# Kernel optimization log

Measured on AMD Instinct MI355X. Metric: run time of the kernel, lower is better.

The kernel has to match this reference:

```python
import jax, jax.numpy as jnp
import numpy as np

BATCH, NODES, CH_IN, CH_OUT, N_EXPERTS = 8, 8192, 128, 128, 64

def setup_inputs() -> dict:
    key = jax.random.key(0)
    kx, kw, ks = jax.random.split(key, 3)
    x = jax.random.normal(kx, (BATCH, NODES, CH_IN), dtype=jnp.float32)
    # std = fan_in**-0.5 per self_init
    W = jax.random.normal(kw, (N_EXPERTS, CH_OUT, CH_IN), dtype=jnp.float32) * (CH_IN ** -0.5)
    sel = jax.random.randint(ks, (NODES,), 0, N_EXPERTS, dtype=jnp.int64)
    return {"x": x, "sel": sel, "W": W}

def reference(x, sel, W):
    # x: (b, n, j), W[sel]: (n, i, j) -> out: (b, n, i)
    Wsel = W[sel]  # gather a (ch_out, ch_in) matrix per node
    return jnp.einsum('bnj,nij->bni', x, Wsel)
```

## Files before the change

kernel.cpp:

```cpp
#include <hip/hip_runtime.h>
#include <hip/hip_bf16.h>

#define BATCH   8
#define NODES   8192
#define CH      128
#define NEXP    64
#define TN      16
#define MAXP    (NODES + NEXP * TN)
#define NTILES  (MAXP / TN)

typedef __attribute__((ext_vector_type(8))) short bf16x8;
typedef __attribute__((ext_vector_type(4))) float f32x4;

__device__ __forceinline__ short f2bf(float f) {
    union { float f; unsigned u; } v; v.f = f;
    unsigned r = (v.u + 0x7fffu + ((v.u >> 16) & 1u)) >> 16;
    return (short)r;
}

__device__ __forceinline__ bf16x8 cvt8(f32x4 lo, f32x4 hi) {
    bf16x8 r;
    r[0] = f2bf(lo[0]); r[1] = f2bf(lo[1]); r[2] = f2bf(lo[2]); r[3] = f2bf(lo[3]);
    r[4] = f2bf(hi[0]); r[5] = f2bf(hi[1]); r[6] = f2bf(hi[2]); r[7] = f2bf(hi[3]);
    return r;
}

__global__ __launch_bounds__(256)
void prep_kernel(const int* __restrict__ sel, const float* __restrict__ W,
                 short* __restrict__ Wbf, int* __restrict__ sorted)
{
    const int e = blockIdx.x;
    const int t = threadIdx.x;

    {
        const float* ws = W   + (size_t)e * CH * CH;
        short*       wd = Wbf + (size_t)e * CH * CH;
        #pragma unroll
        for (int i = 0; i < 8; ++i) {
            int idx = (i * 256 + t) * 8;
            f32x4 lo = *reinterpret_cast<const f32x4*>(ws + idx);
            f32x4 hi = *reinterpret_cast<const f32x4*>(ws + idx + 4);
            *reinterpret_cast<bf16x8*>(wd + idx) = cvt8(lo, hi);
        }
    }

    __shared__ int cnt[NEXP];
    __shared__ int s_off, s_cnt, cursor;
    if (t < NEXP) cnt[t] = 0;
    if (t == 0) cursor = 0;
    __syncthreads();

    int myv[NODES / 256];
    #pragma unroll
    for (int i = 0; i < NODES / 256; ++i) {
        myv[i] = sel[i * 256 + t];
        atomicAdd(&cnt[myv[i]], 1);
    }
    __syncthreads();

    if (t == 0) {
        int off = 0, myoff = 0;
        for (int ee = 0; ee < NEXP; ++ee) {
            if (ee == e) myoff = off;
            off += (cnt[ee] + TN - 1) & ~(TN - 1);
        }
        s_off = myoff;
        s_cnt = cnt[e];
    }
    __syncthreads();

    const int off = s_off, myc = s_cnt;
    const int pad = (myc + TN - 1) & ~(TN - 1);

    for (int i = myc + t; i < pad; i += 256) sorted[off + i] = -1;

    if (e == NEXP - 1) {
        for (int i = off + pad + t; i < MAXP; i += 256) sorted[i] = -1;
    }

    #pragma unroll
    for (int i = 0; i < NODES / 256; ++i) {
        if (myv[i] == e) {
            int pos = atomicAdd(&cursor, 1);
            sorted[off + pos] = i * 256 + t;
        }
    }
}

__global__ __launch_bounds__(256)
void gemm_kernel(const float* __restrict__ x, const int* __restrict__ sel,
                 const short* __restrict__ Wbf, float* __restrict__ out,
                 const int* __restrict__ sorted)
{
    __shared__ int s_nodes[TN];
    __shared__ int s_expert;

    const int tid  = threadIdx.x;
    const int tile = blockIdx.x;

    if (tid < TN) s_nodes[tid] = sorted[tile * TN + tid];
    if (tid == 0) {
        int n0 = sorted[tile * TN];
        s_expert = (n0 >= 0) ? sel[n0] : -1;
    }
    __syncthreads();

    const int e = s_expert;
    if (e < 0) return;

    const int wave = tid >> 6;
    const int lane = tid & 63;
    const int m16  = lane & 15;
    const int quad = lane >> 4;

    const float* xrow[2];
    #pragma unroll
    for (int rt = 0; rt < 2; ++rt) {
        int r    = wave * 32 + rt * 16 + m16;
        int node = s_nodes[r >> 3];
        int b    = r & 7;
        int nd   = (node >= 0) ? node : 0;
        xrow[rt] = x + ((size_t)(b * NODES + nd)) * CH;
    }
    const short* wbase = Wbf + (size_t)e * CH * CH;

    f32x4 acc[2][8];
    #pragma unroll
    for (int rt = 0; rt < 2; ++rt)
        #pragma unroll
        for (int ct = 0; ct < 8; ++ct)
            acc[rt][ct] = (f32x4){0.f, 0.f, 0.f, 0.f};

    #pragma unroll
    for (int kk = 0; kk < 4; ++kk) {
        const int k0 = kk * 32 + quad * 8;

        bf16x8 afrag[2];
        #pragma unroll
        for (int rt = 0; rt < 2; ++rt) {
            const float* p = xrow[rt] + k0;
            f32x4 lo = *reinterpret_cast<const f32x4*>(p);
            f32x4 hi = *reinterpret_cast<const f32x4*>(p + 4);
            afrag[rt] = cvt8(lo, hi);
        }

        #pragma unroll
        for (int ct = 0; ct < 8; ++ct) {
            bf16x8 bfrag = *reinterpret_cast<const bf16x8*>(
                wbase + (size_t)(ct * 16 + m16) * CH + k0);
            acc[0][ct] = __builtin_amdgcn_mfma_f32_16x16x32_bf16(
                             afrag[0], bfrag, acc[0][ct], 0, 0, 0);
            acc[1][ct] = __builtin_amdgcn_mfma_f32_16x16x32_bf16(
                             afrag[1], bfrag, acc[1][ct], 0, 0, 0);
        }
    }

    #pragma unroll
    for (int rt = 0; rt < 2; ++rt) {
        #pragma unroll
        for (int reg = 0; reg < 4; ++reg) {
            int r    = wave * 32 + rt * 16 + quad * 4 + reg;
            int node = s_nodes[r >> 3];
            if (node < 0) continue;
            int b = r & 7;
            float* orow = out + ((size_t)(b * NODES + node)) * CH;
            #pragma unroll
            for (int ct = 0; ct < 8; ++ct)
                orow[ct * 16 + m16] = acc[rt][ct][reg];
        }
    }
}

extern "C" void kernel_launch(void* const* d_in, const int* in_sizes, int n_in,
                              void* d_out, int out_size, void* d_ws, size_t ws_size,
                              hipStream_t stream)
{
    const float* x   = (const float*)d_in[0];
    const int*   sel = (const int*)  d_in[1];
    const float* W   = (const float*)d_in[2];
    float*       out = (float*)d_out;

    short* Wbf   = (short*)d_ws;
    int*   sorted = (int*)((char*)d_ws + (size_t)NEXP * CH * CH * sizeof(short));

    prep_kernel<<<NEXP, 256, 0, stream>>>(sel, W, Wbf, sorted);
    gemm_kernel<<<NTILES, 256, 0, stream>>>(x, sel, Wbf, out, sorted);
}
```

Baseline: 114.4 us.

## Spread weight conversion over more blocks, parallel-scan offsets, and use 512-thread GEMM tiles

The prep kernel now launches 256 blocks so the fp32-to-bf16 weight conversion is spread across more CUs. Per-wave histograms cut LDS atomic contention, and a wave-level shuffle scan replaces the serial offset loop. The GEMM kernel uses 8 waves of 16 rows each instead of 4 waves of 32 rows, which halves per-thread accumulator registers and adds parallelism. Scalar rounding is replaced by the compiler's __bf16 conversion, which may lower to hardware convert instructions. Each B fragment is now reused for one MFMA instead of two, so more waves load the same weight data.

After: 124.3 us. +8.7%, slower.

```diff
diff --git a/kernel.cpp b/kernel.cpp
--- a/kernel.cpp
+++ b/kernel.cpp
@@ -1,5 +1,4 @@
 #include <hip/hip_runtime.h>
-#include <hip/hip_bf16.h>
 
 #define BATCH   8
 #define NODES   8192
@@ -12,16 +11,13 @@
 typedef __attribute__((ext_vector_type(8))) short bf16x8;
 typedef __attribute__((ext_vector_type(4))) float f32x4;
 
-__device__ __forceinline__ short f2bf(float f) {
-    union { float f; unsigned u; } v; v.f = f;
-    unsigned r = (v.u + 0x7fffu + ((v.u >> 16) & 1u)) >> 16;
-    return (short)r;
-}
-
 __device__ __forceinline__ bf16x8 cvt8(f32x4 lo, f32x4 hi) {
     bf16x8 r;
-    r[0] = f2bf(lo[0]); r[1] = f2bf(lo[1]); r[2] = f2bf(lo[2]); r[3] = f2bf(lo[3]);
-    r[4] = f2bf(hi[0]); r[5] = f2bf(hi[1]); r[6] = f2bf(hi[2]); r[7] = f2bf(hi[3]);
+    #pragma unroll
+    for (int i = 0; i < 4; ++i) {
+        r[i]     = (short)__builtin_bit_cast(unsigned short, static_cast<__bf16>(lo[i]));
+        r[i + 4] = (short)__builtin_bit_cast(unsigned short, static_cast<__bf16>(hi[i]));
+    }
     return r;
 }
 
@@ -29,14 +25,14 @@
 void prep_kernel(const int* __restrict__ sel, const float* __restrict__ W,
                  short* __restrict__ Wbf, int* __restrict__ sorted)
 {
-    const int e = blockIdx.x;
     const int t = threadIdx.x;
 
     {
-        const float* ws = W   + (size_t)e * CH * CH;
-        short*       wd = Wbf + (size_t)e * CH * CH;
+        const size_t base = (size_t)blockIdx.x * (CH * CH / 4);
+        const float* ws = W   + base;
+        short*       wd = Wbf + base;
         #pragma unroll
-        for (int i = 0; i < 8; ++i) {
+        for (int i = 0; i < 2; ++i) {
             int idx = (i * 256 + t) * 8;
             f32x4 lo = *reinterpret_cast<const f32x4*>(ws + idx);
             f32x4 hi = *reinterpret_cast<const f32x4*>(ws + idx + 4);
@@ -44,9 +40,13 @@
         }
     }
 
-    __shared__ int cnt[NEXP];
-    __shared__ int s_off, s_cnt, cursor;
-    if (t < NEXP) cnt[t] = 0;
+    const int e = blockIdx.x;
+    if (e >= NEXP) return;
+
+    const int wv = t >> 6;
+    __shared__ int wcnt[4][NEXP];
+    __shared__ int s_off, s_cnt, s_total, cursor;
+    if (t < NEXP) { wcnt[0][t] = 0; wcnt[1][t] = 0; wcnt[2][t] = 0; wcnt[3][t] = 0; }
     if (t == 0) cursor = 0;
     __syncthreads();
 
@@ -54,18 +54,21 @@
     #pragma unroll
     for (int i = 0; i < NODES / 256; ++i) {
         myv[i] = sel[i * 256 + t];
-        atomicAdd(&cnt[myv[i]], 1);
+        atomicAdd(&wcnt[wv][myv[i]], 1);
     }
     __syncthreads();
 
-    if (t == 0) {
-        int off = 0, myoff = 0;
-        for (int ee = 0; ee < NEXP; ++ee) {
-            if (ee == e) myoff = off;
-            off += (cnt[ee] + TN - 1) & ~(TN - 1);
+    if (t < NEXP) {
+        int c = wcnt[0][t] + wcnt[1][t] + wcnt[2][t] + wcnt[3][t];
+        int p = (c + TN - 1) & ~(TN - 1);
+        int scan = p;
+        #pragma unroll
+        for (int d = 1; d < NEXP; d <<= 1) {
+            int v = __shfl_up(scan, d);
+            if (t >= d) scan += v;
         }
-        s_off = myoff;
-        s_cnt = cnt[e];
+        if (t == e)        { s_off = scan - p; s_cnt = c; }
+        if (t == NEXP - 1) s_total = scan;
     }
     __syncthreads();
 
@@ -75,7 +78,7 @@
     for (int i = myc + t; i < pad; i += 256) sorted[off + i] = -1;
 
     if (e == NEXP - 1) {
-        for (int i = off + pad + t; i < MAXP; i += 256) sorted[i] = -1;
+        for (int i = s_total + t; i < MAXP; i += 256) sorted[i] = -1;
     }
 
     #pragma unroll
@@ -87,7 +90,7 @@
     }
 }
 
-__global__ __launch_bounds__(256)
+__global__ __launch_bounds__(512)
 void gemm_kernel(const float* __restrict__ x, const int* __restrict__ sel,
                  const short* __restrict__ Wbf, float* __restrict__ out,
                  const int* __restrict__ sorted)
@@ -113,61 +116,44 @@
     const int m16  = lane & 15;
     const int quad = lane >> 4;
 
-    const float* xrow[2];
-    #pragma unroll
-    for (int rt = 0; rt < 2; ++rt) {
-        int r    = wave * 32 + rt * 16 + m16;
-        int node = s_nodes[r >> 3];
-        int b    = r & 7;
-        int nd   = (node >= 0) ? node : 0;
-        xrow[rt] = x + ((size_t)(b * NODES + nd)) * CH;
-    }
+    const int r    = wave * 16 + m16;
+    const int node = s_nodes[r >> 3];
+    const int b    = r & 7;
+    const int nd   = (node >= 0) ? node : 0;
+    const float* xrow  = x + ((size_t)(b * NODES + nd)) * CH;
     const short* wbase = Wbf + (size_t)e * CH * CH;
 
-    f32x4 acc[2][8];
+    f32x4 acc[8];
     #pragma unroll
-    for (int rt = 0; rt < 2; ++rt)
-        #pragma unroll
-        for (int ct = 0; ct < 8; ++ct)
-            acc[rt][ct] = (f32x4){0.f, 0.f, 0.f, 0.f};
+    for (int ct = 0; ct < 8; ++ct) acc[ct] = (f32x4){0.f, 0.f, 0.f, 0.f};
 
     #pragma unroll
     for (int kk = 0; kk < 4; ++kk) {
         const int k0 = kk * 32 + quad * 8;
 
-        bf16x8 afrag[2];
-        #pragma unroll
-        for (int rt = 0; rt < 2; ++rt) {
-            const float* p = xrow[rt] + k0;
-            f32x4 lo = *reinterpret_cast<const f32x4*>(p);
-            f32x4 hi = *reinterpret_cast<const f32x4*>(p + 4);
-            afrag[rt] = cvt8(lo, hi);
-        }
+        f32x4 lo = *reinterpret_cast<const f32x4*>(xrow + k0);
+        f32x4 hi = *reinterpret_cast<const f32x4*>(xrow + k0 + 4);
+        bf16x8 afrag = cvt8(lo, hi);
 
         #pragma unroll
         for (int ct = 0; ct < 8; ++ct) {
             bf16x8 bfrag = *reinterpret_cast<const bf16x8*>(
                 wbase + (size_t)(ct * 16 + m16) * CH + k0);
-            acc[0][ct] = __builtin_amdgcn_mfma_f32_16x16x32_bf16(
-                             afrag[0], bfrag, acc[0][ct], 0, 0, 0);
-            acc[1][ct] = __builtin_amdgcn_mfma_f32_16x16x32_bf16(
-                             afrag[1], bfrag, acc[1][ct], 0, 0, 0);
+            acc[ct] = __builtin_amdgcn_mfma_f32_16x16x32_bf16(
+                          afrag, bfrag, acc[ct], 0, 0, 0);
         }
     }
 
     #pragma unroll
-    for (int rt = 0; rt < 2; ++rt) {
+    for (int reg = 0; reg < 4; ++reg) {
+        int rr = wave * 16 + quad * 4 + reg;
+        int nn = s_nodes[rr >> 3];
+        if (nn < 0) continue;
+        int bb = rr & 7;
+        float* orow = out + ((size_t)(bb * NODES + nn)) * CH;
         #pragma unroll
-        for (int reg = 0; reg < 4; ++reg) {
-            int r    = wave * 32 + rt * 16 + quad * 4 + reg;
-            int node = s_nodes[r >> 3];
-            if (node < 0) continue;
-            int b = r & 7;
-            float* orow = out + ((size_t)(b * NODES + node)) * CH;
-            #pragma unroll
-            for (int ct = 0; ct < 8; ++ct)
-                orow[ct * 16 + m16] = acc[rt][ct][reg];
-        }
+        for (int ct = 0; ct < 8; ++ct)
+            orow[ct * 16 + m16] = acc[ct][reg];
     }
 }
 
@@ -180,9 +166,9 @@
     const float* W   = (const float*)d_in[2];
     float*       out = (float*)d_out;
 
-    short* Wbf   = (short*)d_ws;
+    short* Wbf    = (short*)d_ws;
     int*   sorted = (int*)((char*)d_ws + (size_t)NEXP * CH * CH * sizeof(short));
 
-    prep_kernel<<<NEXP, 256, 0, stream>>>(sel, W, Wbf, sorted);
-    gemm_kernel<<<NTILES, 256, 0, stream>>>(x, sel, Wbf, out, sorted);
+    prep_kernel<<<256, 256, 0, stream>>>(sel, W, Wbf, sorted);
+    gemm_kernel<<<NTILES, 512, 0, stream>>>(x, sel, Wbf, out, sorted);
 }
```
